# Performance work log

Measured on AMD Instinct MI355X. Metric: run time of the kernel, lower is better.

Reference implementation:

```python
import jax, jax.numpy as jnp
import numpy as np
import math

IN_SIZE = 512
OUT_SIZE = 512
N_HEADS = 8
D_K = OUT_SIZE // N_HEADS  # 64
N_NTYPES = 4
N_ETYPES = 8
MAX_LEN = 240
E = 150000


def _sinusoid_table():
    # RelTemporalEncoding fixed (non-trainable) embedding table [MAX_LEN, IN_SIZE]
    position = np.arange(0.0, MAX_LEN, dtype=np.float64)[:, None]
    div_term = np.exp(np.arange(0, IN_SIZE, 2, dtype=np.float64) * -(math.log(10000.0) / IN_SIZE))
    emb = np.zeros((MAX_LEN, IN_SIZE), dtype=np.float64)
    emb[:, 0::2] = np.sin(position * div_term) / IN_SIZE ** 0.5
    emb[:, 1::2] = np.cos(position * div_term) / IN_SIZE ** 0.5
    return jnp.asarray(emb, dtype=jnp.float32)


def typed_linear(x, types, W, b=None):
    """x: [E, ..., in], types: int[E], W: [T, out, in], b: [T, out] or None.
    Small fixed loop over T types with masked accumulation (avoids gathering a
    huge [E, out, in] weight tensor)."""
    out = jnp.zeros(x.shape[:-1] + (W.shape[1],), x.dtype)
    t_exp = types.reshape((-1,) + (1,) * (x.ndim - 1))
    for t in range(W.shape[0]):
        y = jnp.einsum('...i,oi->...o', x, W[t])
        if b is not None:
            y = y + b[t]
        out = out + jnp.where(t_exp == t, y, jnp.zeros((), x.dtype))
    return out


def setup_inputs() -> dict:
    key = jax.random.key(0)
    ks = jax.random.split(key, 12)
    xavier = lambda k, shape, fan_in, fan_out: jax.random.uniform(
        k, shape, jnp.float32, -1.0, 1.0) * math.sqrt(6.0 / (fan_in + fan_out))
    inp = {
        'h_s': jax.random.normal(ks[0], (E, IN_SIZE), jnp.float32),
        'Q_t': jax.random.normal(ks[1], (E, N_HEADS, D_K), jnp.float32),
        'etype': jax.random.randint(ks[2], (E,), 0, N_ETYPES),
        'tau_s': jax.random.randint(ks[3], (E,), 0, N_NTYPES),
        'dt': jax.random.randint(ks[4], (E,), 0, MAX_LEN),
        # RelTemporalEncoding params
        'emb': _sinusoid_table(),  # fixed, non-trainable
        'lin_W': xavier(ks[5], (IN_SIZE, IN_SIZE), IN_SIZE, IN_SIZE),
        'lin_b': jnp.zeros((IN_SIZE,), jnp.float32),
        # TypedLinear params (xavier_uniform like the torch code)
        'K_W': xavier(ks[6], (N_NTYPES, OUT_SIZE, IN_SIZE), IN_SIZE, OUT_SIZE),
        'K_b': jnp.zeros((N_NTYPES, OUT_SIZE), jnp.float32),
        'V_W': xavier(ks[7], (N_NTYPES, OUT_SIZE, IN_SIZE), IN_SIZE, OUT_SIZE),
        'V_b': jnp.zeros((N_NTYPES, OUT_SIZE), jnp.float32),
        'Watt_W': xavier(ks[8], (N_ETYPES, D_K, D_K), D_K, D_K),
        'Wmsg_W': xavier(ks[9], (N_ETYPES, D_K, D_K), D_K, D_K),
        'mu': jnp.ones((N_ETYPES, N_HEADS), jnp.float32),
    }
    return inp


def reference(h_s, Q_t, etype, tau_s, dt, emb, lin_W, lin_b,
              K_W, K_b, V_W, V_b, Watt_W, Wmsg_W, mu):
    n_edges = h_s.shape[0]
    # RelTemporalEncoding: x + Linear(emb[t])
    h_hat = h_s + emb[dt] @ lin_W.T + lin_b  # [E, in]
    # Typed K/V projections by source node type
    K_s = typed_linear(h_hat, tau_s, K_W, K_b).reshape(n_edges, N_HEADS, D_K)
    V_s = typed_linear(h_hat, tau_s, V_W, V_b).reshape(n_edges, N_HEADS, D_K)
    # Typed per-edge-type transforms
    M = typed_linear(V_s, etype, Wmsg_W)          # [E, H, d_k]
    att_head_k = typed_linear(K_s, etype, Watt_W)  # [E, H, d_k]
    att_head = (Q_t * att_head_k).sum(-1)          # [E, H]
    att_head = att_head * mu[etype] / D_K ** 0.5
    return att_head, M
```

## Files before the change

kernel.cpp:

```cpp
#include <hip/hip_runtime.h>
#include <hip/hip_bf16.h>
#include <stdint.h>

#define E_N 150000
#define IN 512
#define MAXLEN 240

#define PPERM 154112
#define NTILE2 1204
#define GRID_GEMM (NTILE2 * 8)

typedef __attribute__((ext_vector_type(8))) short short8;
typedef __attribute__((ext_vector_type(4))) float f32x4;

#define OFF_RB   0UL
#define OFF_W2   245760UL
#define OFF_B2   33800192UL
#define OFF_RW   33931264UL
#define OFF_CNT  65388544UL
#define OFF_PERM 65389056UL

static __device__ __forceinline__ short f2bf(float f) {
  union { float f; uint32_t u; } v; v.f = f;
  uint32_t u = v.u;
  uint32_t r = (u + 0x7fffu + ((u >> 16) & 1u)) >> 16;
  return (short)r;
}

static __device__ __forceinline__ uint32_t pk2(float a, float b) {
  union { __hip_bfloat162 h; uint32_t u; } v;
  v.h = __float22bfloat162_rn(make_float2(a, b));
  return v.u;
}

__global__ __launch_bounds__(256) void k_rte(const float* __restrict__ emb,
    const float* __restrict__ linW, const float* __restrict__ linB,
    short* __restrict__ Rbf) {
  __shared__ float x[IN];
  int p = blockIdx.x;
  for (int i = threadIdx.x; i < IN; i += 256) x[i] = emb[p * IN + i];
  __syncthreads();
  for (int o = threadIdx.x; o < IN; o += 256) {
    const float* w = linW + (long)o * IN;
    float s = 0.f;
#pragma unroll 4
    for (int k = 0; k < IN; k += 4) {
      float4 wv = *(const float4*)(w + k);
      s += wv.x * x[k] + wv.y * x[k + 1] + wv.z * x[k + 2] + wv.w * x[k + 3];
    }
    Rbf[p * IN + o] = f2bf(s + linB[o]);
  }
}

__global__ __launch_bounds__(256) void k_wpair(
    const float* __restrict__ WattW, const float* __restrict__ WmsgW,
    const float* __restrict__ KW, const float* __restrict__ VW,
    const float* __restrict__ Kb, const float* __restrict__ Vb,
    short* __restrict__ W2, float* __restrict__ B2) {
  __shared__ float Tl[64][65];
  int blk = blockIdx.x;
  int p = blk >> 4, s = blk & 15;
  int t = p >> 3, g = p & 7;
  bool kside = s < 8;
  int h = kside ? s : s - 8;
  const float* T = (kside ? WattW : WmsgW) + (size_t)g * 4096;
  const float* S = (kside ? KW : VW) + ((size_t)t * 512 + h * 64) * 512;
  const float* bsrc = (kside ? Kb : Vb) + t * 512 + h * 64;
  int tid = threadIdx.x;
  for (int i = tid; i < 4096; i += 256) Tl[i >> 6][i & 63] = T[i];
  __syncthreads();
  int op = tid & 63, iq = tid >> 6;
  size_t obase = ((size_t)p * 1024 + (kside ? 0 : 512) + h * 64 + op) * 512;
  for (int i8 = 0; i8 < 16; i8++) {
    int i0 = iq * 128 + i8 * 8;
    float a0 = 0, a1 = 0, a2 = 0, a3 = 0, a4 = 0, a5 = 0, a6 = 0, a7 = 0;
    const float* sp0 = S + i0;
#pragma unroll 8
    for (int j = 0; j < 64; j++) {
      float tv = Tl[op][j];
      const float* sp = sp0 + j * 512;
      float4 s0 = *(const float4*)sp;
      float4 s1 = *(const float4*)(sp + 4);
      a0 += tv * s0.x; a1 += tv * s0.y; a2 += tv * s0.z; a3 += tv * s0.w;
      a4 += tv * s1.x; a5 += tv * s1.y; a6 += tv * s1.z; a7 += tv * s1.w;
    }
    short8 o8;
    o8[0] = f2bf(a0); o8[1] = f2bf(a1); o8[2] = f2bf(a2); o8[3] = f2bf(a3);
    o8[4] = f2bf(a4); o8[5] = f2bf(a5); o8[6] = f2bf(a6); o8[7] = f2bf(a7);
    *(short8*)(W2 + obase + i0) = o8;
  }
  if (tid < 64) {
    float b = 0;
#pragma unroll 8
    for (int j = 0; j < 64; j++) b += Tl[tid][j] * bsrc[j];
    B2[p * 1024 + (kside ? 0 : 512) + h * 64 + tid] = b;
  }
}

__global__ __launch_bounds__(256, 4) void k_rw2(
    const short* __restrict__ Rbf, const short* __restrict__ W2,
    const float* __restrict__ B2, float* __restrict__ RW) {
  __shared__ short sA[4096];
  __shared__ short sB[4096];
  int tid = threadIdx.x;
  int bid = blockIdx.x;
  int p = bid >> 4, rt = (bid >> 3) & 1, ctile = bid & 7;
  int n0 = ctile * 128;
  int r0 = rt * 128;

  int lane = tid & 63, w = tid >> 6, wm = w >> 1, wn = w & 1;

  int rS = w * 32 + (lane >> 2);
  int cS = lane & 3;
  int ch0 = (cS - (rS >> 1)) & 3;
  int ch1 = (cS - ((rS + 16) >> 1)) & 3;
  const char* rbb = (const char*)Rbf;
  const char* srcA0 = rbb + (size_t)(r0 + rS) * 1024 + ch0 * 16;
  const char* srcA1 = rbb + (size_t)(r0 + rS + 16) * 1024 + ch1 * 16;
  const char* wcb = (const char*)(W2 + ((size_t)p * 1024 + n0) * 512);
  const char* srcB0 = wcb + (size_t)rS * 1024 + ch0 * 16;
  const char* srcB1 = wcb + (size_t)(rS + 16) * 1024 + ch1 * 16;
  char* dA0 = (char*)sA + w * 2048;
  char* dA1 = (char*)sA + w * 2048 + 1024;
  char* dB0 = (char*)sB + w * 2048;
  char* dB1 = (char*)sB + w * 2048 + 1024;

  int aRow = wm * 64 + (lane & 15);
  int aOff = aRow * 64 + ((((lane >> 4) + (aRow >> 1)) & 3) << 4);
  int bRow = wn * 64 + (lane & 15);
  int bOff = bRow * 64 + ((((lane >> 4) + (bRow >> 1)) & 3) << 4);

  f32x4 acc[4][4] = {};
#pragma unroll
  for (int kk = 0; kk < 16; kk++) {
    __syncthreads();
    __builtin_amdgcn_global_load_lds((const uint32_t*)(srcA0 + kk * 64), (uint32_t*)dA0, 16, 0, 0);
    __builtin_amdgcn_global_load_lds((const uint32_t*)(srcA1 + kk * 64), (uint32_t*)dA1, 16, 0, 0);
    __builtin_amdgcn_global_load_lds((const uint32_t*)(srcB0 + kk * 64), (uint32_t*)dB0, 16, 0, 0);
    __builtin_amdgcn_global_load_lds((const uint32_t*)(srcB1 + kk * 64), (uint32_t*)dB1, 16, 0, 0);
    __syncthreads();
    short8 a[4], b[4];
#pragma unroll
    for (int mi = 0; mi < 4; mi++)
      a[mi] = *(const short8*)((const char*)sA + aOff + mi * 1024);
#pragma unroll
    for (int ni = 0; ni < 4; ni++)
      b[ni] = *(const short8*)((const char*)sB + bOff + ni * 1024);
#pragma unroll
    for (int mi = 0; mi < 4; mi++)
#pragma unroll
      for (int ni = 0; ni < 4; ni++)
        acc[mi][ni] = __builtin_amdgcn_mfma_f32_16x16x32_bf16(a[mi], b[ni], acc[mi][ni], 0, 0, 0);
  }

  int l15 = lane & 15;
  int rbase = (lane >> 4) * 4;
  float bias[4];
#pragma unroll
  for (int ni = 0; ni < 4; ni++)
    bias[ni] = B2[p * 1024 + n0 + wn * 64 + ni * 16 + l15];
#pragma unroll
  for (int mi = 0; mi < 4; mi++) {
#pragma unroll
    for (int r = 0; r < 4; r++) {
      int row = r0 + wm * 64 + mi * 16 + rbase + r;
      if (row >= MAXLEN) continue;
      float* dst = RW + ((size_t)p * 240 + row) * 1024 + n0 + wn * 64;
#pragma unroll
      for (int ni = 0; ni < 4; ni++)
        dst[ni * 16 + l15] = acc[mi][ni][r] + bias[ni];
    }
  }
}

__global__ __launch_bounds__(256) void k_hist(const int* __restrict__ tau,
    const int* __restrict__ et, int* __restrict__ cnt) {
  __shared__ int l[32];
  if (threadIdx.x < 32) l[threadIdx.x] = 0;
  __syncthreads();
  int e = blockIdx.x * 256 + threadIdx.x;
  if (e < E_N) atomicAdd(&l[tau[e] * 8 + et[e]], 1);
  __syncthreads();
  if (threadIdx.x < 32) atomicAdd(&cnt[threadIdx.x], l[threadIdx.x]);
}

__global__ void k_bases(int* c) {
  int b = 0;
  for (int p = 0; p < 32; p++) {
    c[32 + p] = b;
    b += ((c[p] + 127) >> 7) << 7;
    c[64 + p] = 0;
  }
}

__global__ __launch_bounds__(256) void k_scatter(const int* __restrict__ tau,
    const int* __restrict__ et, int* __restrict__ c, int* __restrict__ perm) {
  __shared__ int lc[32], lbase[32];
  if (threadIdx.x < 32) lc[threadIdx.x] = 0;
  __syncthreads();
  int e = blockIdx.x * 256 + threadIdx.x;
  bool v = e < E_N;
  int cls = 0, pos = 0;
  if (v) {
    cls = tau[e] * 8 + et[e];
    pos = atomicAdd(&lc[cls], 1);
  }
  __syncthreads();
  if (threadIdx.x < 32) {
    int n = lc[threadIdx.x];
    lbase[threadIdx.x] = (n > 0) ? atomicAdd(&c[64 + threadIdx.x], n) : 0;
  }
  __syncthreads();
  if (v) perm[c[32 + cls] + lbase[cls] + pos] = e;
}

__global__ __launch_bounds__(256, 4) void k_gemm(
    const float* __restrict__ hs, const int* __restrict__ dt,
    const int* __restrict__ tau, const int* __restrict__ et,
    const short* __restrict__ W2, const float* __restrict__ RW,
    const float* __restrict__ Qt, const float* __restrict__ mu,
    const int* __restrict__ perm,
    float* __restrict__ Mout, float* __restrict__ attOut) {
  __shared__ short sA[128][40];
  __shared__ short sB[4096];
  __shared__ int eRow[128];
  __shared__ int dtRow[128];
  __shared__ int metaP;
  int tid = threadIdx.x;
  int l = (blockIdx.x & 7) * NTILE2 + (blockIdx.x >> 3);
  int ttile = l >> 3, ctile = l & 7;
  int m0 = ttile * 128;
  if (tid < 128) {
    int e = perm[m0 + tid];
    eRow[tid] = e;
    dtRow[tid] = (e >= 0) ? dt[e] : 0;
  }
  if (tid == 0) {
    int e0 = perm[m0];
    metaP = (e0 >= 0) ? (tau[e0] * 8 + et[e0]) : -1;
  }
  __syncthreads();
  int p = metaP;
  if (p < 0) return;
  int n0 = ctile * 128;

  int lane = tid & 63, w = tid >> 6, wm = w >> 1, wn = w & 1;

  int arow = tid >> 1;
  int ahalf = tid & 1;
  long aE = eRow[arow]; if (aE < 0) aE = 0;
  const float* asrc = hs + aE * 512 + ahalf * 16;

  int rS = w * 32 + (lane >> 2);
  int cS = lane & 3;
  int ch0 = (cS - (rS >> 1)) & 3;
  int ch1 = (cS - ((rS + 16) >> 1)) & 3;
  const char* wcb = (const char*)(W2 + ((size_t)p * 1024 + n0) * 512);
  const char* srcB0 = wcb + (size_t)rS * 1024 + ch0 * 16;
  const char* srcB1 = wcb + (size_t)(rS + 16) * 1024 + ch1 * 16;
  char* dB0 = (char*)sB + w * 2048;
  char* dB1 = (char*)sB + w * 2048 + 1024;

  int aRowF = wm * 64 + (lane & 15);
  int lk8 = (lane >> 4) * 8;
  int bRow = wn * 64 + (lane & 15);
  int bOff = bRow * 64 + ((((lane >> 4) + (bRow >> 1)) & 3) << 4);

  f32x4 acc[4][4] = {};
  float4 pf0 = *(const float4*)(asrc);
  float4 pf1 = *(const float4*)(asrc + 4);
  float4 pf2 = *(const float4*)(asrc + 8);
  float4 pf3 = *(const float4*)(asrc + 12);
#pragma unroll
  for (int kk = 0; kk < 16; kk++) {
    __syncthreads();
    union { short8 s; uint32_t u[4]; } w0, w1;
    w0.u[0] = pk2(pf0.x, pf0.y); w0.u[1] = pk2(pf0.z, pf0.w);
    w0.u[2] = pk2(pf1.x, pf1.y); w0.u[3] = pk2(pf1.z, pf1.w);
    w1.u[0] = pk2(pf2.x, pf2.y); w1.u[1] = pk2(pf2.z, pf2.w);
    w1.u[2] = pk2(pf3.x, pf3.y); w1.u[3] = pk2(pf3.z, pf3.w);
    *(short8*)&sA[arow][ahalf * 16] = w0.s;
    *(short8*)&sA[arow][ahalf * 16 + 8] = w1.s;
    __builtin_amdgcn_global_load_lds((const uint32_t*)(srcB0 + kk * 64), (uint32_t*)dB0, 16, 0, 0);
    __builtin_amdgcn_global_load_lds((const uint32_t*)(srcB1 + kk * 64), (uint32_t*)dB1, 16, 0, 0);
    if (kk < 15) {
      const float* np = asrc + (kk + 1) * 32;
      pf0 = *(const float4*)(np);
      pf1 = *(const float4*)(np + 4);
      pf2 = *(const float4*)(np + 8);
      pf3 = *(const float4*)(np + 12);
    }
    __syncthreads();
    short8 a[4], b[4];
#pragma unroll
    for (int mi = 0; mi < 4; mi++)
      a[mi] = *(const short8*)&sA[aRowF + mi * 16][lk8];
#pragma unroll
    for (int ni = 0; ni < 4; ni++)
      b[ni] = *(const short8*)((const char*)sB + bOff + ni * 1024);
#pragma unroll
    for (int mi = 0; mi < 4; mi++)
#pragma unroll
      for (int ni = 0; ni < 4; ni++)
        acc[mi][ni] = __builtin_amdgcn_mfma_f32_16x16x32_bf16(a[mi], b[ni], acc[mi][ni], 0, 0, 0);
  }

  int l15 = lane & 15;
  int rbase = (lane >> 4) * 4;
  if (ctile < 4) {
    int h = ctile * 2 + wn;
    float muv = mu[(p & 7) * 8 + h] * 0.125f;
#pragma unroll
    for (int mi = 0; mi < 4; mi++) {
#pragma unroll
      for (int r = 0; r < 4; r++) {
        int row = wm * 64 + mi * 16 + rbase + r;
        int e = eRow[row];
        if (e < 0) continue;
        const float* rw = RW + ((size_t)p * 240 + dtRow[row]) * 1024 + n0 + wn * 64;
        const float* qp = Qt + (size_t)e * 512 + h * 64;
        float s = 0.f;
#pragma unroll
        for (int ni = 0; ni < 4; ni++)
          s += qp[ni * 16 + l15] * (acc[mi][ni][r] + rw[ni * 16 + l15]);
        s += __shfl_xor(s, 1);
        s += __shfl_xor(s, 2);
        s += __shfl_xor(s, 4);
        s += __shfl_xor(s, 8);
        if (l15 == 0) attOut[(size_t)e * 8 + h] = s * muv;
      }
    }
  } else {
#pragma unroll
    for (int mi = 0; mi < 4; mi++) {
#pragma unroll
      for (int r = 0; r < 4; r++) {
        int row = wm * 64 + mi * 16 + rbase + r;
        int e = eRow[row];
        if (e < 0) continue;
        const float* rw = RW + ((size_t)p * 240 + dtRow[row]) * 1024 + n0 + wn * 64;
        float* md = Mout + (size_t)e * 512 + (n0 - 512) + wn * 64;
#pragma unroll
        for (int ni = 0; ni < 4; ni++)
          md[ni * 16 + l15] = acc[mi][ni][r] + rw[ni * 16 + l15];
      }
    }
  }
}

extern "C" void kernel_launch(void* const* d_in, const int* in_sizes, int n_in,
                              void* d_out, int out_size, void* d_ws, size_t ws_size,
                              hipStream_t stream) {
  const float* hs    = (const float*)d_in[0];
  const float* Qt    = (const float*)d_in[1];
  const int*   et    = (const int*)d_in[2];
  const int*   tau   = (const int*)d_in[3];
  const int*   dt    = (const int*)d_in[4];
  const float* emb   = (const float*)d_in[5];
  const float* linW  = (const float*)d_in[6];
  const float* linB  = (const float*)d_in[7];
  const float* KW    = (const float*)d_in[8];
  const float* Kb    = (const float*)d_in[9];
  const float* VW    = (const float*)d_in[10];
  const float* Vb    = (const float*)d_in[11];
  const float* WattW = (const float*)d_in[12];
  const float* WmsgW = (const float*)d_in[13];
  const float* mu    = (const float*)d_in[14];

  char* ws = (char*)d_ws;
  short* Rbf  = (short*)(ws + OFF_RB);
  short* W2   = (short*)(ws + OFF_W2);
  float* B2   = (float*)(ws + OFF_B2);
  float* RW   = (float*)(ws + OFF_RW);
  int*   cnt  = (int*)(ws + OFF_CNT);
  int*   perm = (int*)(ws + OFF_PERM);

  float* attOut = (float*)d_out;
  float* Mout   = (float*)d_out + (long)E_N * 8;

  hipMemsetAsync(cnt, 0, 128 * sizeof(int), stream);
  hipMemsetAsync(perm, 0xFF, PPERM * sizeof(int), stream);

  k_rte<<<240, 256, 0, stream>>>(emb, linW, linB, Rbf);
  k_wpair<<<512, 256, 0, stream>>>(WattW, WmsgW, KW, VW, Kb, Vb, W2, B2);
  k_hist<<<(E_N + 255) / 256, 256, 0, stream>>>(tau, et, cnt);
  k_bases<<<1, 1, 0, stream>>>(cnt);
  k_scatter<<<(E_N + 255) / 256, 256, 0, stream>>>(tau, et, cnt, perm);
  k_rw2<<<512, 256, 0, stream>>>(Rbf, W2, B2, RW);
  k_gemm<<<GRID_GEMM, 256, 0, stream>>>(hs, dt, tau, et, W2, RW, Qt, mu, perm, Mout, attOut);
}
```

Measured before the change: 713.9 us.

## Load GEMM operands directly from global into registers, split weight-pair kernel wider

The main GEMM kernel stops staging A (hs rows converted to bf16) and B (fused weights) through LDS with barriers. Each wave now loads its own MFMA fragments straight from global memory into registers. This removes the syncthreads and LDS traffic, but each element is fetched redundantly by several waves and the global accesses are less coalesced, relying on L1/L2. Separately, the weight-pair precompute kernel is split across 4x more blocks, each handling a quarter of the inner columns, to raise parallelism; occupancy hint drops to 3 blocks per CU.

```diff
diff --git a/kernel.cpp b/kernel.cpp
--- a/kernel.cpp
+++ b/kernel.cpp
@@ -59,7 +59,7 @@
     short* __restrict__ W2, float* __restrict__ B2) {
   __shared__ float Tl[64][65];
   int blk = blockIdx.x;
-  int p = blk >> 4, s = blk & 15;
+  int p = blk >> 6, s = (blk >> 2) & 15, q = blk & 3;
   int t = p >> 3, g = p & 7;
   bool kside = s < 8;
   int h = kside ? s : s - 8;
@@ -71,7 +71,7 @@
   __syncthreads();
   int op = tid & 63, iq = tid >> 6;
   size_t obase = ((size_t)p * 1024 + (kside ? 0 : 512) + h * 64 + op) * 512;
-  for (int i8 = 0; i8 < 16; i8++) {
+  for (int i8 = q * 4; i8 < q * 4 + 4; i8++) {
     int i0 = iq * 128 + i8 * 8;
     float a0 = 0, a1 = 0, a2 = 0, a3 = 0, a4 = 0, a5 = 0, a6 = 0, a7 = 0;
     const float* sp0 = S + i0;
@@ -89,7 +89,7 @@
     o8[4] = f2bf(a4); o8[5] = f2bf(a5); o8[6] = f2bf(a6); o8[7] = f2bf(a7);
     *(short8*)(W2 + obase + i0) = o8;
   }
-  if (tid < 64) {
+  if (q == 0 && tid < 64) {
     float b = 0;
 #pragma unroll 8
     for (int j = 0; j < 64; j++) b += Tl[tid][j] * bsrc[j];
@@ -214,15 +214,13 @@
   if (v) perm[c[32 + cls] + lbase[cls] + pos] = e;
 }
 
-__global__ __launch_bounds__(256, 4) void k_gemm(
+__global__ __launch_bounds__(256, 3) void k_gemm(
     const float* __restrict__ hs, const int* __restrict__ dt,
     const int* __restrict__ tau, const int* __restrict__ et,
     const short* __restrict__ W2, const float* __restrict__ RW,
     const float* __restrict__ Qt, const float* __restrict__ mu,
     const int* __restrict__ perm,
     float* __restrict__ Mout, float* __restrict__ attOut) {
-  __shared__ short sA[128][40];
-  __shared__ short sB[4096];
   __shared__ int eRow[128];
   __shared__ int dtRow[128];
   __shared__ int metaP;
@@ -245,59 +243,34 @@
   int n0 = ctile * 128;
 
   int lane = tid & 63, w = tid >> 6, wm = w >> 1, wn = w & 1;
-
-  int arow = tid >> 1;
-  int ahalf = tid & 1;
-  long aE = eRow[arow]; if (aE < 0) aE = 0;
-  const float* asrc = hs + aE * 512 + ahalf * 16;
-
-  int rS = w * 32 + (lane >> 2);
-  int cS = lane & 3;
-  int ch0 = (cS - (rS >> 1)) & 3;
-  int ch1 = (cS - ((rS + 16) >> 1)) & 3;
-  const char* wcb = (const char*)(W2 + ((size_t)p * 1024 + n0) * 512);
-  const char* srcB0 = wcb + (size_t)rS * 1024 + ch0 * 16;
-  const char* srcB1 = wcb + (size_t)(rS + 16) * 1024 + ch1 * 16;
-  char* dB0 = (char*)sB + w * 2048;
-  char* dB1 = (char*)sB + w * 2048 + 1024;
-
-  int aRowF = wm * 64 + (lane & 15);
-  int lk8 = (lane >> 4) * 8;
-  int bRow = wn * 64 + (lane & 15);
-  int bOff = bRow * 64 + ((((lane >> 4) + (bRow >> 1)) & 3) << 4);
+  int l15 = lane & 15;
+  int kg = lane >> 4;
+
+  const float* aP[4];
+#pragma unroll
+  for (int mi = 0; mi < 4; mi++) {
+    int e = eRow[wm * 64 + mi * 16 + l15];
+    if (e < 0) e = 0;
+    aP[mi] = hs + (size_t)e * 512 + kg * 8;
+  }
+  const short* bP = W2 + ((size_t)p * 1024 + n0 + wn * 64 + l15) * 512 + kg * 8;
 
   f32x4 acc[4][4] = {};
-  float4 pf0 = *(const float4*)(asrc);
-  float4 pf1 = *(const float4*)(asrc + 4);
-  float4 pf2 = *(const float4*)(asrc + 8);
-  float4 pf3 = *(const float4*)(asrc + 12);
-#pragma unroll
+#pragma unroll 2
   for (int kk = 0; kk < 16; kk++) {
-    __syncthreads();
-    union { short8 s; uint32_t u[4]; } w0, w1;
-    w0.u[0] = pk2(pf0.x, pf0.y); w0.u[1] = pk2(pf0.z, pf0.w);
-    w0.u[2] = pk2(pf1.x, pf1.y); w0.u[3] = pk2(pf1.z, pf1.w);
-    w1.u[0] = pk2(pf2.x, pf2.y); w1.u[1] = pk2(pf2.z, pf2.w);
-    w1.u[2] = pk2(pf3.x, pf3.y); w1.u[3] = pk2(pf3.z, pf3.w);
-    *(short8*)&sA[arow][ahalf * 16] = w0.s;
-    *(short8*)&sA[arow][ahalf * 16 + 8] = w1.s;
-    __builtin_amdgcn_global_load_lds((const uint32_t*)(srcB0 + kk * 64), (uint32_t*)dB0, 16, 0, 0);
-    __builtin_amdgcn_global_load_lds((const uint32_t*)(srcB1 + kk * 64), (uint32_t*)dB1, 16, 0, 0);
-    if (kk < 15) {
-      const float* np = asrc + (kk + 1) * 32;
-      pf0 = *(const float4*)(np);
-      pf1 = *(const float4*)(np + 4);
-      pf2 = *(const float4*)(np + 8);
-      pf3 = *(const float4*)(np + 12);
-    }
-    __syncthreads();
     short8 a[4], b[4];
 #pragma unroll
-    for (int mi = 0; mi < 4; mi++)
-      a[mi] = *(const short8*)&sA[aRowF + mi * 16][lk8];
+    for (int mi = 0; mi < 4; mi++) {
+      float4 f0 = *(const float4*)(aP[mi] + kk * 32);
+      float4 f1 = *(const float4*)(aP[mi] + kk * 32 + 4);
+      union { short8 s; uint32_t u[4]; } t;
+      t.u[0] = pk2(f0.x, f0.y); t.u[1] = pk2(f0.z, f0.w);
+      t.u[2] = pk2(f1.x, f1.y); t.u[3] = pk2(f1.z, f1.w);
+      a[mi] = t.s;
+    }
 #pragma unroll
     for (int ni = 0; ni < 4; ni++)
-      b[ni] = *(const short8*)((const char*)sB + bOff + ni * 1024);
+      b[ni] = *(const short8*)(bP + (size_t)ni * 16 * 512 + kk * 32);
 #pragma unroll
     for (int mi = 0; mi < 4; mi++)
 #pragma unroll
@@ -305,7 +278,6 @@
         acc[mi][ni] = __builtin_amdgcn_mfma_f32_16x16x32_bf16(a[mi], b[ni], acc[mi][ni], 0, 0, 0);
   }
 
-  int l15 = lane & 15;
   int rbase = (lane >> 4) * 4;
   if (ctile < 4) {
     int h = ctile * 2 + wn;
@@ -382,7 +354,7 @@
   hipMemsetAsync(perm, 0xFF, PPERM * sizeof(int), stream);
 
   k_rte<<<240, 256, 0, stream>>>(emb, linW, linB, Rbf);
-  k_wpair<<<512, 256, 0, stream>>>(WattW, WmsgW, KW, VW, Kb, Vb, W2, B2);
+  k_wpair<<<2048, 256, 0, stream>>>(WattW, WmsgW, KW, VW, Kb, Vb, W2, B2);
   k_hist<<<(E_N + 255) / 256, 256, 0, stream>>>(tau, et, cnt);
   k_bases<<<1, 1, 0, stream>>>(cnt);
   k_scatter<<<(E_N + 255) / 256, 256, 0, stream>>>(tau, et, cnt, perm);
```

Result: slower. 1.133 ms (+58.7%).
